# Performance work log

Measured on AMD Instinct MI355X. Metric: run time of the kernel, lower is better.

Reference implementation:

```python
import jax, jax.numpy as jnp
import numpy as np

B, D, H, W, C = 8, 24, 24, 24, 192
NH = 6
WS = (4, 4, 4)
SS = (2, 2, 2)
HIDDEN = 4 * C
CPB_H = 512


def _buffers():
    wd, wh, ww = WS
    rd = np.arange(-(wd - 1), wd, dtype=np.float32)
    rh = np.arange(-(wh - 1), wh, dtype=np.float32)
    rw = np.arange(-(ww - 1), ww, dtype=np.float32)
    table = np.stack(np.meshgrid(rd, rh, rw, indexing='ij'), axis=-1)[None]  # (1,2wd-1,2wh-1,2ww-1,3)
    table[..., 0] /= (wd - 1)
    table[..., 1] /= (wh - 1)
    table[..., 2] /= (ww - 1)
    table *= 8.0
    table = np.sign(table) * np.log2(np.abs(table) + 1.0) / np.log2(8.0)
    coords = np.stack(np.meshgrid(np.arange(wd), np.arange(wh), np.arange(ww), indexing='ij'))
    cf = coords.reshape(3, -1)
    rel = (cf[:, :, None] - cf[:, None, :]).transpose(1, 2, 0).astype(np.int64)
    rel[..., 0] += wd - 1
    rel[..., 1] += wh - 1
    rel[..., 2] += ww - 1
    rel[..., 0] *= (2 * wh - 1) * (2 * ww - 1)
    rel[..., 1] *= (2 * ww - 1)
    return table.astype(np.float32), rel.sum(-1).astype(np.int32)


def _attn_mask():
    wd, wh, ww = WS
    img = np.zeros((1, D, H, W, 1), np.float32)
    cnt = 0
    def sl(w, s):
        return (slice(0, -w), slice(-w, -s), slice(-s, None))
    for d_ in sl(wd, SS[0]):
        for h_ in sl(wh, SS[1]):
            for w_ in sl(ww, SS[2]):
                img[:, d_, h_, w_, :] = cnt
                cnt += 1
    mw = img.reshape(1, D // wd, wd, H // wh, wh, W // ww, ww, 1)
    mw = mw.transpose(0, 1, 3, 5, 2, 4, 6, 7).reshape(-1, wd * wh * ww)  # (nW, N)
    am = mw[:, None, :] - mw[:, :, None]
    return np.where(am != 0, -100.0, 0.0).astype(np.float32)


def setup_inputs() -> dict:
    key = jax.random.key(0)
    ks = jax.random.split(key, 8)
    w = lambda k, shape: jax.random.normal(k, shape, jnp.float32) * 0.02
    table, rpi = _buffers()
    return {
        'x': jax.random.normal(ks[0], (B, D, H, W, C), jnp.float32),
        'norm1_w': jnp.ones((C,), jnp.float32), 'norm1_b': jnp.zeros((C,), jnp.float32),
        'qkv_w': w(ks[1], (3 * C, C)),
        'q_bias': jnp.zeros((C,), jnp.float32), 'v_bias': jnp.zeros((C,), jnp.float32),
        'logit_scale': jnp.log(10.0) * jnp.ones((NH, 1, 1), jnp.float32),
        'cpb_w1': w(ks[2], (CPB_H, 3)), 'cpb_b1': jnp.zeros((CPB_H,), jnp.float32),
        'cpb_w2': w(ks[3], (NH, CPB_H)),
        'proj_w': w(ks[4], (C, C)), 'proj_b': jnp.zeros((C,), jnp.float32),
        'norm2_w': jnp.ones((C,), jnp.float32), 'norm2_b': jnp.zeros((C,), jnp.float32),
        'fc1_w': w(ks[5], (HIDDEN, C)), 'fc1_b': jnp.zeros((HIDDEN,), jnp.float32),
        'fc2_w': w(ks[6], (C, HIDDEN)), 'fc2_b': jnp.zeros((C,), jnp.float32),
        'rel_table': jnp.asarray(table),
        'rel_index': jnp.asarray(rpi),
        'attn_mask': jnp.asarray(_attn_mask()),
    }


def _ln(x, w, b):
    mu = x.mean(-1, keepdims=True)
    var = ((x - mu) ** 2).mean(-1, keepdims=True)
    return (x - mu) * jax.lax.rsqrt(var + 1e-5) * w + b


def _forward(x, norm1_w, norm1_b, qkv_w, q_bias, v_bias, logit_scale,
             cpb_w1, cpb_b1, cpb_w2, proj_w, proj_b, norm2_w, norm2_b,
             fc1_w, fc1_b, fc2_w, fc2_b, rel_table, rel_index, attn_mask):
    wd, wh, ww = WS
    N = wd * wh * ww
    hd = C // NH
    shortcut = x
    h = _ln(x, norm1_w, norm1_b)
    h = jnp.roll(h, (-SS[0], -SS[1], -SS[2]), axis=(1, 2, 3))
    # window partition -> (B*nW, N, C)
    xw = h.reshape(B, D // wd, wd, H // wh, wh, W // ww, ww, C)
    xw = xw.transpose(0, 1, 3, 5, 2, 4, 6, 7).reshape(-1, N, C)
    B_ = xw.shape[0]
    # NOTE: faithful to torch source, where qkv is recomputed via self.qkv(x)
    # (bias=False), discarding the assembled qkv_bias. q_bias/v_bias thus unused.
    qkv = (xw @ qkv_w.T).reshape(B_, N, 3, NH, hd).transpose(2, 0, 3, 1, 4)
    q, k, v = qkv[0], qkv[1], qkv[2]  # each (B_, NH, N, hd)
    qn = q / jnp.maximum(jnp.linalg.norm(q, axis=-1, keepdims=True), 1e-12)
    kn = k / jnp.maximum(jnp.linalg.norm(k, axis=-1, keepdims=True), 1e-12)
    attn = jnp.einsum('bhnd,bhmd->bhnm', qn, kn)
    scale = jnp.exp(jnp.minimum(logit_scale, jnp.log(100.0)))  # (NH,1,1)
    attn = attn * scale
    # continuous position bias MLP -> gather per relative index
    bias_table = jax.nn.relu(rel_table.reshape(-1, 3) @ cpb_w1.T + cpb_b1) @ cpb_w2.T  # (T, NH)
    rpb = bias_table[rel_index.reshape(-1)].reshape(N, N, NH).transpose(2, 0, 1)
    attn = attn + 16.0 * jax.nn.sigmoid(rpb)[None]
    nW = attn_mask.shape[0]
    attn = attn.reshape(B_ // nW, nW, NH, N, N) + attn_mask[None, :, None]
    attn = jax.nn.softmax(attn.reshape(B_, NH, N, N), axis=-1)
    out = jnp.einsum('bhnm,bhmd->bhnd', attn, v).transpose(0, 2, 1, 3).reshape(B_, N, C)
    out = out @ proj_w.T + proj_b
    # window reverse -> (B, D, H, W, C)
    out = out.reshape(B, D // wd, H // wh, W // ww, wd, wh, ww, C)
    out = out.transpose(0, 1, 4, 2, 5, 3, 6, 7).reshape(B, D, H, W, C)
    out = jnp.roll(out, (SS[0], SS[1], SS[2]), axis=(1, 2, 3))
    h = shortcut + out
    m = _ln(h, norm2_w, norm2_b)
    m = jax.nn.gelu(m @ fc1_w.T + fc1_b, approximate=False)
    m = m @ fc2_w.T + fc2_b
    return h + m


def reference(x, norm1_w, norm1_b, qkv_w, q_bias, v_bias, logit_scale,
              cpb_w1, cpb_b1, cpb_w2, proj_w, proj_b, norm2_w, norm2_b,
              fc1_w, fc1_b, fc2_w, fc2_b, rel_table, rel_index, attn_mask):
    return _forward(x, norm1_w, norm1_b, qkv_w, q_bias, v_bias, logit_scale,
                    cpb_w1, cpb_b1, cpb_w2, proj_w, proj_b, norm2_w, norm2_b,
                    fc1_w, fc1_b, fc2_w, fc2_b, rel_table, rel_index, attn_mask)
```

## Files before the change

kernel.cpp:

```cpp
#include <hip/hip_runtime.h>
#include <hip/hip_bf16.h>
#include <math.h>

typedef __attribute__((ext_vector_type(8))) short bf16x8;
typedef __attribute__((ext_vector_type(4))) float f32x4;

__device__ inline ushort f2bf(float f) {
    __hip_bfloat16 h = __float2bfloat16(f);
    return *reinterpret_cast<ushort*>(&h);
}
__device__ inline float bf2f(ushort u) {
    return __uint_as_float(((unsigned int)u) << 16);
}

__global__ __launch_bounds__(256) void k_cpb_table(
        const float* __restrict__ rtab, const float* __restrict__ w1,
        const float* __restrict__ b1, const float* __restrict__ w2,
        float* __restrict__ table_out) {
    int idx = blockIdx.x * 256 + threadIdx.x;
    if (idx >= 343 * 6) return;
    int r = idx / 6, head = idx - r * 6;
    float t0 = rtab[r*3+0], t1 = rtab[r*3+1], t2 = rtab[r*3+2];
    float s = 0.f;
    for (int j = 0; j < 512; ++j) {
        float a = t0*w1[j*3+0] + t1*w1[j*3+1] + t2*w1[j*3+2] + b1[j];
        a = fmaxf(a, 0.f);
        s += a * w2[head*512 + j];
    }
    table_out[idx] = s;
}

__global__ __launch_bounds__(256) void k_bias16(
        const float* __restrict__ table_out, const int* __restrict__ ridx,
        float* __restrict__ bias16) {
    int idx = blockIdx.x * 256 + threadIdx.x;
    if (idx >= 6 * 64 * 64) return;
    int head = idx >> 12;
    int nm = idx & 4095;
    float v = table_out[ridx[nm] * 6 + head];
    bias16[idx] = 16.f / (1.f + expf(-v));
}

__global__ __launch_bounds__(256) void k_wcvt(
        const float* __restrict__ qkvw, const float* __restrict__ f1w,
        const float* __restrict__ f2w, const float* __restrict__ pw,
        ushort* __restrict__ Wqb, ushort* __restrict__ W1b,
        ushort* __restrict__ W2b, ushort* __restrict__ Wpb) {
    int i = blockIdx.x * 256 + threadIdx.x;
    W1b[i] = f2bf(f1w[i]);
    W2b[i] = f2bf(f2w[i]);
    if (i < 110592) Wqb[i] = f2bf(qkvw[i]);
    if (i < 36864)  Wpb[i] = f2bf(pw[i]);
}

__global__ __launch_bounds__(256) void k_ln1(
        const float* __restrict__ x, const float* __restrict__ nw,
        const float* __restrict__ nb, ushort* __restrict__ buf1) {
    const int wb = blockIdx.x;
    const int b = wb / 216, win = wb - b * 216;
    const int wdi = win / 36, whi = (win / 6) % 6, wwi = win % 6;
    const int t = threadIdx.x;
    const int n = t >> 2, sub = t & 3;
    const int id = n >> 4, ih = (n >> 2) & 3, iw = n & 3;
    const int dsrc = (wdi*4 + id + 2) % 24;
    const int hsrc = (whi*4 + ih + 2) % 24;
    const int wsrc = (wwi*4 + iw + 2) % 24;
    const float* xr = x + (size_t)(((b*24 + dsrc)*24 + hsrc)*24 + wsrc) * 192 + sub*48;
    float4 q[12];
    float sum = 0.f, ssum = 0.f;
    #pragma unroll
    for (int j = 0; j < 12; ++j) {
        q[j] = reinterpret_cast<const float4*>(xr)[j];
        sum  += q[j].x + q[j].y + q[j].z + q[j].w;
        ssum += q[j].x*q[j].x + q[j].y*q[j].y + q[j].z*q[j].z + q[j].w*q[j].w;
    }
    sum  += __shfl_xor(sum, 1);  sum  += __shfl_xor(sum, 2);
    ssum += __shfl_xor(ssum, 1); ssum += __shfl_xor(ssum, 2);
    float mu = sum * (1.f/192.f);
    float inv = rsqrtf(ssum * (1.f/192.f) - mu*mu + 1e-5f);
    ushort* op = buf1 + ((size_t)wb*64 + n)*192 + sub*48;
    #pragma unroll
    for (int j = 0; j < 12; ++j) {
        int c = sub*48 + j*4;
        ushort4 o;
        o.x = f2bf((q[j].x - mu)*inv*nw[c+0] + nb[c+0]);
        o.y = f2bf((q[j].y - mu)*inv*nw[c+1] + nb[c+1]);
        o.z = f2bf((q[j].z - mu)*inv*nw[c+2] + nb[c+2]);
        o.w = f2bf((q[j].w - mu)*inv*nw[c+3] + nb[c+3]);
        *reinterpret_cast<ushort4*>(op + j*4) = o;
    }
}

__global__ __launch_bounds__(256) void k_attn3(
        const ushort* __restrict__ buf1, const ushort* __restrict__ Wqb,
        const float* __restrict__ ls, const float* __restrict__ bias16,
        const float* __restrict__ amask, ushort* __restrict__ buf2) {
    __shared__ ushort QK[2][3][64][40];
    __shared__ ushort Vt[3][32][72];
    __shared__ ushort Pl[4][16][72];
    const int wb = blockIdx.x;
    const int win = wb % 216;
    const int t = threadIdx.x;
    const int wid = t >> 6, lane = t & 63;
    const int fr = lane & 15, fg = lane >> 4;
    const int trow = wid * 16;
    const ushort* Abase = buf1 + (size_t)wb * 12288 + (size_t)(trow + fr) * 192 + fg * 8;

    for (int g = 0; g < 2; ++g) {
        if (g) __syncthreads();
        f32x4 acc[18] = {};
        #pragma unroll
        for (int ks = 0; ks < 6; ++ks) {
            bf16x8 a = *(const bf16x8*)(Abase + ks*32);
            #pragma unroll
            for (int ct = 0; ct < 18; ++ct) {
                const int seg = ct / 6, u = ct % 6;
                const int gcol = seg*192 + g*96 + u*16;
                bf16x8 b = *(const bf16x8*)(Wqb + (size_t)(gcol + fr)*192 + ks*32 + fg*8);
                acc[ct] = __builtin_amdgcn_mfma_f32_16x16x32_bf16(a, b, acc[ct], 0, 0, 0);
            }
        }
        #pragma unroll
        for (int ct = 0; ct < 18; ++ct) {
            const int seg = ct / 6, u = ct % 6;
            const int hl = u >> 1, dp = u & 1;
            if (seg < 2) {
                #pragma unroll
                for (int e = 0; e < 4; ++e)
                    QK[seg][hl][trow + fg*4 + e][dp*16 + fr] = f2bf(acc[ct][e]);
            } else {
                ushort4 v4;
                v4.x = f2bf(acc[ct][0]); v4.y = f2bf(acc[ct][1]);
                v4.z = f2bf(acc[ct][2]); v4.w = f2bf(acc[ct][3]);
                *reinterpret_cast<ushort4*>(&Vt[hl][dp*16 + fr][trow + fg*4]) = v4;
            }
        }
        __syncthreads();
        {
            float scq[3];
            #pragma unroll
            for (int hl = 0; hl < 3; ++hl)
                scq[hl] = expf(fminf(ls[g*3 + hl], 4.6051701859880914f));
            for (int rr = t; rr < 384; rr += 256) {
                const int mat = rr / 192, rem = rr - mat*192;
                const int hl = rem >> 6, n = rem & 63;
                ushort* p = &QK[mat][hl][n][0];
                float vals[32];
                float ss = 0.f;
                #pragma unroll
                for (int j = 0; j < 8; ++j) {
                    ushort4 u4 = *reinterpret_cast<const ushort4*>(p + j*4);
                    float a0 = bf2f(u4.x), a1 = bf2f(u4.y), a2 = bf2f(u4.z), a3 = bf2f(u4.w);
                    vals[j*4+0]=a0; vals[j*4+1]=a1; vals[j*4+2]=a2; vals[j*4+3]=a3;
                    ss += a0*a0 + a1*a1 + a2*a2 + a3*a3;
                }
                float f = 1.f / fmaxf(sqrtf(ss), 1e-12f);
                if (mat == 0) f *= (hl == 0 ? scq[0] : (hl == 1 ? scq[1] : scq[2]));
                #pragma unroll
                for (int j = 0; j < 8; ++j) {
                    ushort4 o;
                    o.x = f2bf(vals[j*4+0]*f); o.y = f2bf(vals[j*4+1]*f);
                    o.z = f2bf(vals[j*4+2]*f); o.w = f2bf(vals[j*4+3]*f);
                    *reinterpret_cast<ushort4*>(p + j*4) = o;
                }
            }
        }
        __syncthreads();
        #pragma unroll 1
        for (int hl = 0; hl < 3; ++hl) {
            const int h = g*3 + hl;
            bf16x8 qf = *(const bf16x8*)&QK[0][hl][trow + fr][fg*8];
            f32x4 accS[4] = {};
            #pragma unroll
            for (int j = 0; j < 4; ++j) {
                bf16x8 kf = *(const bf16x8*)&QK[1][hl][j*16 + fr][fg*8];
                accS[j] = __builtin_amdgcn_mfma_f32_16x16x32_bf16(qf, kf, accS[j], 0, 0, 0);
            }
            float s[4][4];
            const float* bi = bias16 + h*4096;
            const float* mk = amask + (size_t)win*4096;
            #pragma unroll
            for (int e = 0; e < 4; ++e) {
                const int r = trow + fg*4 + e;
                #pragma unroll
                for (int j = 0; j < 4; ++j) {
                    const int c = j*16 + fr;
                    s[j][e] = accS[j][e] + bi[r*64 + c] + mk[r*64 + c];
                }
            }
            #pragma unroll
            for (int e = 0; e < 4; ++e) {
                float m0 = fmaxf(fmaxf(s[0][e], s[1][e]), fmaxf(s[2][e], s[3][e]));
                m0 = fmaxf(m0, __shfl_xor(m0, 1));
                m0 = fmaxf(m0, __shfl_xor(m0, 2));
                m0 = fmaxf(m0, __shfl_xor(m0, 4));
                m0 = fmaxf(m0, __shfl_xor(m0, 8));
                float s0 = 0.f;
                #pragma unroll
                for (int j = 0; j < 4; ++j) { s[j][e] = expf(s[j][e] - m0); s0 += s[j][e]; }
                s0 += __shfl_xor(s0, 1);
                s0 += __shfl_xor(s0, 2);
                s0 += __shfl_xor(s0, 4);
                s0 += __shfl_xor(s0, 8);
                const float rs = 1.f / s0;
                #pragma unroll
                for (int j = 0; j < 4; ++j)
                    Pl[wid][fg*4 + e][j*16 + fr] = f2bf(s[j][e] * rs);
            }
            f32x4 accO[2] = {};
            #pragma unroll
            for (int kk = 0; kk < 2; ++kk) {
                bf16x8 pa = *(const bf16x8*)&Pl[wid][fr][kk*32 + fg*8];
                #pragma unroll
                for (int j = 0; j < 2; ++j) {
                    bf16x8 vb = *(const bf16x8*)&Vt[hl][j*16 + fr][kk*32 + fg*8];
                    accO[j] = __builtin_amdgcn_mfma_f32_16x16x32_bf16(pa, vb, accO[j], 0, 0, 0);
                }
            }
            #pragma unroll
            for (int j = 0; j < 2; ++j) {
                #pragma unroll
                for (int e = 0; e < 4; ++e) {
                    buf2[(size_t)wb*12288 + (size_t)(trow + fg*4 + e)*192 + h*32 + j*16 + fr]
                        = f2bf(accO[j][e]);
                }
            }
        }
    }
}

__global__ __launch_bounds__(256) void k_proj(
        const ushort* __restrict__ buf2, const float* __restrict__ x,
        const ushort* __restrict__ Wpb, const float* __restrict__ pb,
        float* __restrict__ out) {
    __shared__ ushort As[64 * 200];
    __shared__ int rowbase[64];
    const int t = threadIdx.x;
    const size_t base = (size_t)blockIdx.x * 64;
    if (t < 64) {
        int dst = (int)base + t;
        int b = dst / 13824, r1 = dst - b * 13824;
        int d = r1 / 576, h2 = (r1 / 24) % 24, w2 = r1 % 24;
        int dd = (d + 22) % 24, hh = (h2 + 22) % 24, ww = (w2 + 22) % 24;
        int win = ((dd >> 2)*6 + (hh >> 2))*6 + (ww >> 2);
        int n = ((dd & 3) << 4) | ((hh & 3) << 2) | (ww & 3);
        rowbase[t] = ((b*216 + win)*64 + n) * 192;
    }
    __syncthreads();
    {
        const int r = t >> 2, q = t & 3;
        const ushort* src = buf2 + rowbase[r] + q*48;
        #pragma unroll
        for (int i = 0; i < 6; ++i)
            *(bf16x8*)(As + r*200 + q*48 + i*8) = *(const bf16x8*)(src + i*8);
    }
    __syncthreads();

    const int wid = t >> 6, lane = t & 63;
    const int fr = lane & 15, fg = lane >> 4;
    const int trow = wid * 16;
    f32x4 acc[12] = {};
    #pragma unroll
    for (int ks = 0; ks < 6; ++ks) {
        bf16x8 a = *(const bf16x8*)(As + (trow + fr)*200 + ks*32 + fg*8);
        #pragma unroll
        for (int j = 0; j < 12; ++j) {
            bf16x8 b = *(const bf16x8*)(Wpb + (size_t)(j*16 + fr)*192 + ks*32 + fg*8);
            acc[j] = __builtin_amdgcn_mfma_f32_16x16x32_bf16(a, b, acc[j], 0, 0, 0);
        }
    }
    #pragma unroll
    for (int j = 0; j < 12; ++j) {
        int c = j*16 + fr;
        float bias = pb[c];
        #pragma unroll
        for (int e = 0; e < 4; ++e) {
            size_t idx = (base + trow + fg*4 + e)*192 + c;
            out[idx] = x[idx] + acc[j][e] + bias;
        }
    }
}

__global__ __launch_bounds__(256, 2) void k_mlp3(
        const ushort* __restrict__ W1b, const ushort* __restrict__ W2b,
        const float* __restrict__ n2w, const float* __restrict__ n2b,
        const float* __restrict__ f1b, const float* __restrict__ f2b,
        float* __restrict__ out) {
    __shared__ ushort As[4][32][200];
    __shared__ ushort Hs[4][32][68];
    const int t = threadIdx.x;
    const int wid = t >> 6, lane = t & 63;
    const size_t tok0 = (size_t)blockIdx.x * 128 + wid * 32;

    {
        const int r = lane >> 1, half = lane & 1;
        const float* hp = out + (tok0 + r) * 192 + half * 96;
        float4 v[24];
        float sum = 0.f, ssum = 0.f;
        #pragma unroll
        for (int j = 0; j < 24; ++j) {
            v[j] = reinterpret_cast<const float4*>(hp)[j];
            sum  += v[j].x + v[j].y + v[j].z + v[j].w;
            ssum += v[j].x*v[j].x + v[j].y*v[j].y + v[j].z*v[j].z + v[j].w*v[j].w;
        }
        sum  += __shfl_xor(sum, 1);
        ssum += __shfl_xor(ssum, 1);
        float mu = sum * (1.f/192.f);
        float inv = rsqrtf(ssum * (1.f/192.f) - mu*mu + 1e-5f);
        #pragma unroll
        for (int j = 0; j < 24; ++j) {
            int c = half*96 + j*4;
            ushort4 o;
            o.x = f2bf((v[j].x - mu)*inv*n2w[c+0] + n2b[c+0]);
            o.y = f2bf((v[j].y - mu)*inv*n2w[c+1] + n2b[c+1]);
            o.z = f2bf((v[j].z - mu)*inv*n2w[c+2] + n2b[c+2]);
            o.w = f2bf((v[j].w - mu)*inv*n2w[c+3] + n2b[c+3]);
            *reinterpret_cast<ushort4*>(&As[wid][r][c]) = o;
        }
    }

    const int fr = lane & 15, fg = lane >> 4;
    bf16x8 a[2][6];
    #pragma unroll
    for (int tf = 0; tf < 2; ++tf)
        #pragma unroll
        for (int ks = 0; ks < 6; ++ks)
            a[tf][ks] = *(const bf16x8*)&As[wid][tf*16 + fr][ks*32 + fg*8];

    f32x4 acc2[2][12] = {};

    for (int hb = 0; hb < 768; hb += 64) {
        f32x4 acc1[2][4] = {};
        #pragma unroll
        for (int ks = 0; ks < 6; ++ks) {
            bf16x8 b[4];
            #pragma unroll
            for (int j = 0; j < 4; ++j)
                b[j] = *(const bf16x8*)(W1b + (size_t)(hb + j*16 + fr)*192 + ks*32 + fg*8);
            #pragma unroll
            for (int j = 0; j < 4; ++j) {
                acc1[0][j] = __builtin_amdgcn_mfma_f32_16x16x32_bf16(a[0][ks], b[j], acc1[0][j], 0, 0, 0);
                acc1[1][j] = __builtin_amdgcn_mfma_f32_16x16x32_bf16(a[1][ks], b[j], acc1[1][j], 0, 0, 0);
            }
        }
        #pragma unroll
        for (int j = 0; j < 4; ++j) {
            float bias = f1b[hb + j*16 + fr];
            #pragma unroll
            for (int tf = 0; tf < 2; ++tf) {
                #pragma unroll
                for (int e = 0; e < 4; ++e) {
                    float h = acc1[tf][j][e] + bias;
                    h = 0.5f*h*(1.f + erff(h*0.70710678118654752f));
                    Hs[wid][tf*16 + fg*4 + e][j*16 + fr] = f2bf(h);
                }
            }
        }
        #pragma unroll
        for (int ks2 = 0; ks2 < 2; ++ks2) {
            bf16x8 ha0 = *(const bf16x8*)&Hs[wid][fr][ks2*32 + fg*8];
            bf16x8 ha1 = *(const bf16x8*)&Hs[wid][16 + fr][ks2*32 + fg*8];
            #pragma unroll
            for (int j = 0; j < 12; ++j) {
                bf16x8 b = *(const bf16x8*)(W2b + (size_t)(j*16 + fr)*768 + hb + ks2*32 + fg*8);
                acc2[0][j] = __builtin_amdgcn_mfma_f32_16x16x32_bf16(ha0, b, acc2[0][j], 0, 0, 0);
                acc2[1][j] = __builtin_amdgcn_mfma_f32_16x16x32_bf16(ha1, b, acc2[1][j], 0, 0, 0);
            }
        }
    }

    #pragma unroll
    for (int j = 0; j < 12; ++j) {
        int c = j*16 + fr;
        float bias = f2b[c];
        #pragma unroll
        for (int tf = 0; tf < 2; ++tf) {
            #pragma unroll
            for (int e = 0; e < 4; ++e) {
                size_t idx = (tok0 + tf*16 + fg*4 + e)*192 + c;
                out[idx] += acc2[tf][j][e] + bias;
            }
        }
    }
}

extern "C" void kernel_launch(void* const* d_in, const int* in_sizes, int n_in,
                              void* d_out, int out_size, void* d_ws, size_t ws_size,
                              hipStream_t stream) {
    const float* x     = (const float*)d_in[0];
    const float* n1w   = (const float*)d_in[1];
    const float* n1b   = (const float*)d_in[2];
    const float* qkvw  = (const float*)d_in[3];
    const float* ls    = (const float*)d_in[6];
    const float* cpw1  = (const float*)d_in[7];
    const float* cpb1  = (const float*)d_in[8];
    const float* cpw2  = (const float*)d_in[9];
    const float* pw    = (const float*)d_in[10];
    const float* pb    = (const float*)d_in[11];
    const float* n2w   = (const float*)d_in[12];
    const float* n2b   = (const float*)d_in[13];
    const float* f1w   = (const float*)d_in[14];
    const float* f1b   = (const float*)d_in[15];
    const float* f2w   = (const float*)d_in[16];
    const float* f2b   = (const float*)d_in[17];
    const float* rtab  = (const float*)d_in[18];
    const int*   ridx  = (const int*)d_in[19];
    const float* amask = (const float*)d_in[20];
    float* out = (float*)d_out;

    ushort* buf1 = (ushort*)d_ws;
    ushort* buf2 = buf1 + 21233664;
    ushort* Wqb  = buf2 + 21233664;
    ushort* W1b  = Wqb + 110592;
    ushort* W2b  = W1b + 147456;
    ushort* Wpb  = W2b + 147456;
    float*  tblo = (float*)(Wpb + 36864);
    float*  b16  = tblo + 2064;

    k_cpb_table<<<dim3(9),    dim3(256), 0, stream>>>(rtab, cpw1, cpb1, cpw2, tblo);
    k_bias16   <<<dim3(96),   dim3(256), 0, stream>>>(tblo, ridx, b16);
    k_wcvt     <<<dim3(576),  dim3(256), 0, stream>>>(qkvw, f1w, f2w, pw, Wqb, W1b, W2b, Wpb);
    k_ln1      <<<dim3(1728), dim3(256), 0, stream>>>(x, n1w, n1b, buf1);
    k_attn3    <<<dim3(1728), dim3(256), 0, stream>>>(buf1, Wqb, ls, b16, amask, buf2);
    k_proj     <<<dim3(1728), dim3(256), 0, stream>>>(buf2, x, Wpb, pb, out);
    k_mlp3     <<<dim3(864),  dim3(256), 0, stream>>>(W1b, W2b, n2w, n2b, f1b, f2b, out);
}
```

Baseline: 966.7 us.

## Pre-swizzle bf16 weights into MFMA fragment order and drop LDS staging in MLP

The weight conversion kernel now writes qkv, fc1, fc2 and proj weights in MFMA B-fragment order, so each wave loads one contiguous 1KB chunk per fragment instead of strided rows. The MLP kernel computes LayerNorm directly into A-fragment registers using cross-lane shuffles, which removes the shared-memory As staging buffer. Its occupancy hint is raised from 2 to 4 blocks per CU. The intent is better coalescing of weight loads and less LDS traffic, at the cost of more register pressure under the tighter launch bound.

```diff
diff --git a/kernel.cpp b/kernel.cpp
--- a/kernel.cpp
+++ b/kernel.cpp
@@ -44,13 +44,42 @@
 __global__ __launch_bounds__(256) void k_wcvt(
         const float* __restrict__ qkvw, const float* __restrict__ f1w,
         const float* __restrict__ f2w, const float* __restrict__ pw,
-        ushort* __restrict__ Wqb, ushort* __restrict__ W1b,
-        ushort* __restrict__ W2b, ushort* __restrict__ Wpb) {
-    int i = blockIdx.x * 256 + threadIdx.x;
-    W1b[i] = f2bf(f1w[i]);
-    W2b[i] = f2bf(f2w[i]);
-    if (i < 110592) Wqb[i] = f2bf(qkvw[i]);
-    if (i < 36864)  Wpb[i] = f2bf(pw[i]);
+        ushort* __restrict__ Wqs, ushort* __restrict__ W1s,
+        ushort* __restrict__ W2s, ushort* __restrict__ Wps) {
+    const int i = blockIdx.x * 256 + threadIdx.x;
+    const int l = i & 63, fr = l & 15, fg = l >> 4;
+    const float* src = nullptr;
+    ushort* dst = nullptr;
+    if (i < 18432) {
+        int r = i >> 6;
+        int j = r & 3, r2 = r >> 2;
+        int ks = r2 % 6, c = r2 / 6;
+        src = f1w + (size_t)(c*64 + j*16 + fr)*192 + ks*32 + fg*8;
+        dst = W1s + (size_t)i*8;
+    } else if (i < 36864) {
+        int g2 = i - 18432;
+        int r = g2 >> 6;
+        int j = r % 12, r2 = r / 12;
+        int ks2 = r2 & 1, c = r2 >> 1;
+        src = f2w + (size_t)(j*16 + fr)*768 + c*64 + ks2*32 + fg*8;
+        dst = W2s + (size_t)g2*8;
+    } else if (i < 41472) {
+        int g2 = i - 36864;
+        int r = g2 >> 6;
+        int j = r % 12, ks = r / 12;
+        src = pw + (size_t)(j*16 + fr)*192 + ks*32 + fg*8;
+        dst = Wps + (size_t)g2*8;
+    } else if (i < 55296) {
+        int g2 = i - 41472;
+        int r = g2 >> 6;
+        int ks = r % 6, r2 = r / 6;
+        int ct = r2 % 18, grp = r2 / 18;
+        int seg = ct / 6, u = ct % 6;
+        src = qkvw + (size_t)(seg*192 + grp*96 + u*16 + fr)*192 + ks*32 + fg*8;
+        dst = Wqs + (size_t)g2*8;
+    } else return;
+    #pragma unroll
+    for (int e = 0; e < 8; ++e) dst[e] = f2bf(src[e]);
 }
 
 __global__ __launch_bounds__(256) void k_ln1(
@@ -92,7 +121,7 @@
 }
 
 __global__ __launch_bounds__(256) void k_attn3(
-        const ushort* __restrict__ buf1, const ushort* __restrict__ Wqb,
+        const ushort* __restrict__ buf1, const ushort* __restrict__ Wqs,
         const float* __restrict__ ls, const float* __restrict__ bias16,
         const float* __restrict__ amask, ushort* __restrict__ buf2) {
     __shared__ ushort QK[2][3][64][40];
@@ -114,9 +143,7 @@
             bf16x8 a = *(const bf16x8*)(Abase + ks*32);
             #pragma unroll
             for (int ct = 0; ct < 18; ++ct) {
-                const int seg = ct / 6, u = ct % 6;
-                const int gcol = seg*192 + g*96 + u*16;
-                bf16x8 b = *(const bf16x8*)(Wqb + (size_t)(gcol + fr)*192 + ks*32 + fg*8);
+                bf16x8 b = *(const bf16x8*)(Wqs + ((size_t)((g*18 + ct)*6 + ks)*64 + lane)*8);
                 acc[ct] = __builtin_amdgcn_mfma_f32_16x16x32_bf16(a, b, acc[ct], 0, 0, 0);
             }
         }
@@ -231,7 +258,7 @@
 
 __global__ __launch_bounds__(256) void k_proj(
         const ushort* __restrict__ buf2, const float* __restrict__ x,
-        const ushort* __restrict__ Wpb, const float* __restrict__ pb,
+        const ushort* __restrict__ Wps, const float* __restrict__ pb,
         float* __restrict__ out) {
     __shared__ ushort As[64 * 200];
     __shared__ int rowbase[64];
@@ -265,7 +292,7 @@
         bf16x8 a = *(const bf16x8*)(As + (trow + fr)*200 + ks*32 + fg*8);
         #pragma unroll
         for (int j = 0; j < 12; ++j) {
-            bf16x8 b = *(const bf16x8*)(Wpb + (size_t)(j*16 + fr)*192 + ks*32 + fg*8);
+            bf16x8 b = *(const bf16x8*)(Wps + ((size_t)(ks*12 + j)*64 + lane)*8);
             acc[j] = __builtin_amdgcn_mfma_f32_16x16x32_bf16(a, b, acc[j], 0, 0, 0);
         }
     }
@@ -281,62 +308,65 @@
     }
 }
 
-__global__ __launch_bounds__(256, 2) void k_mlp3(
-        const ushort* __restrict__ W1b, const ushort* __restrict__ W2b,
+__global__ __launch_bounds__(256, 4) void k_mlp3(
+        const ushort* __restrict__ W1s, const ushort* __restrict__ W2s,
         const float* __restrict__ n2w, const float* __restrict__ n2b,
         const float* __restrict__ f1b, const float* __restrict__ f2b,
         float* __restrict__ out) {
-    __shared__ ushort As[4][32][200];
     __shared__ ushort Hs[4][32][68];
     const int t = threadIdx.x;
     const int wid = t >> 6, lane = t & 63;
+    const int fr = lane & 15, fg = lane >> 4;
     const size_t tok0 = (size_t)blockIdx.x * 128 + wid * 32;
 
-    {
-        const int r = lane >> 1, half = lane & 1;
-        const float* hp = out + (tok0 + r) * 192 + half * 96;
-        float4 v[24];
+    bf16x8 a[2][6];
+    #pragma unroll
+    for (int tf = 0; tf < 2; ++tf) {
+        const float* hp = out + (tok0 + tf*16 + fr) * 192 + fg*8;
+        float4 q[12];
         float sum = 0.f, ssum = 0.f;
         #pragma unroll
-        for (int j = 0; j < 24; ++j) {
-            v[j] = reinterpret_cast<const float4*>(hp)[j];
-            sum  += v[j].x + v[j].y + v[j].z + v[j].w;
-            ssum += v[j].x*v[j].x + v[j].y*v[j].y + v[j].z*v[j].z + v[j].w*v[j].w;
-        }
-        sum  += __shfl_xor(sum, 1);
-        ssum += __shfl_xor(ssum, 1);
+        for (int ks = 0; ks < 6; ++ks) {
+            q[ks*2]   = *reinterpret_cast<const float4*>(hp + ks*32);
+            q[ks*2+1] = *reinterpret_cast<const float4*>(hp + ks*32 + 4);
+        }
+        #pragma unroll
+        for (int j = 0; j < 12; ++j) {
+            sum  += q[j].x + q[j].y + q[j].z + q[j].w;
+            ssum += q[j].x*q[j].x + q[j].y*q[j].y + q[j].z*q[j].z + q[j].w*q[j].w;
+        }
+        sum  += __shfl_xor(sum, 16);  sum  += __shfl_xor(sum, 32);
+        ssum += __shfl_xor(ssum, 16); ssum += __shfl_xor(ssum, 32);
         float mu = sum * (1.f/192.f);
         float inv = rsqrtf(ssum * (1.f/192.f) - mu*mu + 1e-5f);
         #pragma unroll
-        for (int j = 0; j < 24; ++j) {
-            int c = half*96 + j*4;
-            ushort4 o;
-            o.x = f2bf((v[j].x - mu)*inv*n2w[c+0] + n2b[c+0]);
-            o.y = f2bf((v[j].y - mu)*inv*n2w[c+1] + n2b[c+1]);
-            o.z = f2bf((v[j].z - mu)*inv*n2w[c+2] + n2b[c+2]);
-            o.w = f2bf((v[j].w - mu)*inv*n2w[c+3] + n2b[c+3]);
-            *reinterpret_cast<ushort4*>(&As[wid][r][c]) = o;
-        }
-    }
-
-    const int fr = lane & 15, fg = lane >> 4;
-    bf16x8 a[2][6];
-    #pragma unroll
-    for (int tf = 0; tf < 2; ++tf)
-        #pragma unroll
-        for (int ks = 0; ks < 6; ++ks)
-            a[tf][ks] = *(const bf16x8*)&As[wid][tf*16 + fr][ks*32 + fg*8];
+        for (int ks = 0; ks < 6; ++ks) {
+            const int c = ks*32 + fg*8;
+            float4 w0 = *reinterpret_cast<const float4*>(n2w + c);
+            float4 w1 = *reinterpret_cast<const float4*>(n2w + c + 4);
+            float4 b0 = *reinterpret_cast<const float4*>(n2b + c);
+            float4 b1 = *reinterpret_cast<const float4*>(n2b + c + 4);
+            a[tf][ks][0] = (short)f2bf((q[ks*2].x   - mu)*inv*w0.x + b0.x);
+            a[tf][ks][1] = (short)f2bf((q[ks*2].y   - mu)*inv*w0.y + b0.y);
+            a[tf][ks][2] = (short)f2bf((q[ks*2].z   - mu)*inv*w0.z + b0.z);
+            a[tf][ks][3] = (short)f2bf((q[ks*2].w   - mu)*inv*w0.w + b0.w);
+            a[tf][ks][4] = (short)f2bf((q[ks*2+1].x - mu)*inv*w1.x + b1.x);
+            a[tf][ks][5] = (short)f2bf((q[ks*2+1].y - mu)*inv*w1.y + b1.y);
+            a[tf][ks][6] = (short)f2bf((q[ks*2+1].z - mu)*inv*w1.z + b1.z);
+            a[tf][ks][7] = (short)f2bf((q[ks*2+1].w - mu)*inv*w1.w + b1.w);
+        }
+    }
 
     f32x4 acc2[2][12] = {};
 
-    for (int hb = 0; hb < 768; hb += 64) {
+    for (int c = 0; c < 12; ++c) {
         f32x4 acc1[2][4] = {};
         #pragma unroll
         for (int ks = 0; ks < 6; ++ks) {
             bf16x8 b[4];
             #pragma unroll
             for (int j = 0; j < 4; ++j)
-                b[j] = *(const bf16x8*)(W1b + (size_t)(hb + j*16 + fr)*192 + ks*32 + fg*8);
+                b[j] = *(const bf16x8*)(W1s + ((size_t)((c*6 + ks)*4 + j)*64 + lane)*8);
             #pragma unroll
             for (int j = 0; j < 4; ++j) {
                 acc1[0][j] = __builtin_amdgcn_mfma_f32_16x16x32_bf16(a[0][ks], b[j], acc1[0][j], 0, 0, 0);
@@ -345,7 +375,7 @@
         }
         #pragma unroll
         for (int j = 0; j < 4; ++j) {
-            float bias = f1b[hb + j*16 + fr];
+            float bias = f1b[c*64 + j*16 + fr];
             #pragma unroll
             for (int tf = 0; tf < 2; ++tf) {
                 #pragma unroll
@@ -362,7 +392,7 @@
             bf16x8 ha1 = *(const bf16x8*)&Hs[wid][16 + fr][ks2*32 + fg*8];
             #pragma unroll
             for (int j = 0; j < 12; ++j) {
-                bf16x8 b = *(const bf16x8*)(W2b + (size_t)(j*16 + fr)*768 + hb + ks2*32 + fg*8);
+                bf16x8 b = *(const bf16x8*)(W2s + ((size_t)((c*2 + ks2)*12 + j)*64 + lane)*8);
                 acc2[0][j] = __builtin_amdgcn_mfma_f32_16x16x32_bf16(ha0, b, acc2[0][j], 0, 0, 0);
                 acc2[1][j] = __builtin_amdgcn_mfma_f32_16x16x32_bf16(ha1, b, acc2[1][j], 0, 0, 0);
             }
@@ -371,13 +401,13 @@
 
     #pragma unroll
     for (int j = 0; j < 12; ++j) {
-        int c = j*16 + fr;
-        float bias = f2b[c];
+        int cch = j*16 + fr;
+        float bias = f2b[cch];
         #pragma unroll
         for (int tf = 0; tf < 2; ++tf) {
             #pragma unroll
             for (int e = 0; e < 4; ++e) {
-                size_t idx = (tok0 + tf*16 + fg*4 + e)*192 + c;
+                size_t idx = (tok0 + tf*16 + fg*4 + e)*192 + cch;
                 out[idx] += acc2[tf][j][e] + bias;
             }
         }
@@ -410,18 +440,18 @@
 
     ushort* buf1 = (ushort*)d_ws;
     ushort* buf2 = buf1 + 21233664;
-    ushort* Wqb  = buf2 + 21233664;
-    ushort* W1b  = Wqb + 110592;
-    ushort* W2b  = W1b + 147456;
-    ushort* Wpb  = W2b + 147456;
-    float*  tblo = (float*)(Wpb + 36864);
+    ushort* Wqs  = buf2 + 21233664;
+    ushort* W1s  = Wqs + 110592;
+    ushort* W2s  = W1s + 147456;
+    ushort* Wps  = W2s + 147456;
+    float*  tblo = (float*)(Wps + 36864);
     float*  b16  = tblo + 2064;
 
     k_cpb_table<<<dim3(9),    dim3(256), 0, stream>>>(rtab, cpw1, cpb1, cpw2, tblo);
     k_bias16   <<<dim3(96),   dim3(256), 0, stream>>>(tblo, ridx, b16);
-    k_wcvt     <<<dim3(576),  dim3(256), 0, stream>>>(qkvw, f1w, f2w, pw, Wqb, W1b, W2b, Wpb);
+    k_wcvt     <<<dim3(216),  dim3(256), 0, stream>>>(qkvw, f1w, f2w, pw, Wqs, W1s, W2s, Wps);
     k_ln1      <<<dim3(1728), dim3(256), 0, stream>>>(x, n1w, n1b, buf1);
-    k_attn3    <<<dim3(1728), dim3(256), 0, stream>>>(buf1, Wqb, ls, b16, amask, buf2);
-    k_proj     <<<dim3(1728), dim3(256), 0, stream>>>(buf2, x, Wpb, pb, out);
-    k_mlp3     <<<dim3(864),  dim3(256), 0, stream>>>(W1b, W2b, n2w, n2b, f1b, f2b, out);
-}
+    k_attn3    <<<dim3(1728), dim3(256), 0, stream>>>(buf1, Wqs, ls, b16, amask, buf2);
+    k_proj     <<<dim3(1728), dim3(256), 0, stream>>>(buf2, x, Wps, pb, out);
+    k_mlp3     <<<dim3(864),  dim3(256), 0, stream>>>(W1s, W2s, n2w, n2b, f1b, f2b, out);
+}
```

New measurement: 990.8 us. +2.5%, slower.
